# Optimization experiments

Measured on AMD Instinct MI355X. Metric: run time of the kernel, lower is better.

The kernel has to match this reference:

```python
import jax, jax.numpy as jnp
import numpy as np


def setup_inputs() -> dict:
    key = jax.random.key(0)
    k = jax.random.split(key, 6)
    B, C = 16, 256
    Hd, Wd = 32, 32   # deeper (lower-res) spatial
    Hs, Ws = 64, 64   # shallower (higher-res) spatial
    deeper = jax.random.normal(k[0], (B, C, Hd, Wd), dtype=jnp.float32)
    shallower = jax.random.normal(k[1], (B, C, Hs, Ws), dtype=jnp.float32)
    # 1x1 conv weights stored as dense matrices (kernel spatial dims are 1)
    w1 = jax.random.normal(k[2], (C, 2 * C), dtype=jnp.float32) * (1.0 / np.sqrt(2 * C))
    b1 = jnp.zeros((C,), dtype=jnp.float32)
    w2 = jax.random.normal(k[3], (C, C), dtype=jnp.float32) * (1.0 / np.sqrt(C))
    b2 = jnp.zeros((C,), dtype=jnp.float32)
    return {"deeper": deeper, "shallower": shallower, "w1": w1, "b1": b1, "w2": w2, "b2": b2}


def reference(deeper, shallower, w1, b1, w2, b2):
    # Global average pools (adaptive_avg_pool2d to 1x1) -> [B, C]
    shallow_pool = jnp.mean(shallower, axis=(2, 3))
    deeper_pool = jnp.mean(deeper, axis=(2, 3))  # deepest=False branch
    # Channel-wise concat -> [B, 2C]
    global_pool = jnp.concatenate([shallow_pool, deeper_pool], axis=1)
    # conv1x1 -> ReLU (LeakyReLU slope 0.0) -> conv1x1, on 1x1 spatial = dense matmuls
    h = jax.nn.relu(jnp.einsum('bi,oi->bo', global_pool, w1) + b1)
    gate = jnp.einsum('bi,oi->bo', h, w2) + b2  # [B, C]
    # Sigmoid channel gating broadcast over spatial dims
    gated = shallower * jax.nn.sigmoid(gate)[:, :, None, None]
    # Bilinear upsample deeper to shallower resolution (align_corners=False)
    B, C, Hs, Ws = shallower.shape
    up = jax.image.resize(deeper, (B, C, Hs, Ws), method='bilinear')
    return gated + up
```

## Files before the change

### kernel.cpp

```cpp
#include <hip/hip_runtime.h>
#include <math.h>


__global__ __launch_bounds__(256) void pool_kernel(const float* __restrict__ deeper,
                                                   const float* __restrict__ shallower,
                                                   float* __restrict__ gp) {
    const int bc = blockIdx.x;
    const int t = threadIdx.x;
    const float4* ssrc = (const float4*)(shallower + (size_t)bc * 4096);
    const float4* dsrc = (const float4*)(deeper + (size_t)bc * 1024);
    float4 a = ssrc[t], b4 = ssrc[t + 256], c4 = ssrc[t + 512], d4 = ssrc[t + 768];
    float4 e = dsrc[t];
    float s_sh = (a.x + a.y + a.z + a.w) + (b4.x + b4.y + b4.z + b4.w)
               + (c4.x + c4.y + c4.z + c4.w) + (d4.x + d4.y + d4.z + d4.w);
    float s_dp = e.x + e.y + e.z + e.w;
    #pragma unroll
    for (int off = 32; off > 0; off >>= 1) {
        s_sh += __shfl_down(s_sh, off, 64);
        s_dp += __shfl_down(s_dp, off, 64);
    }
    __shared__ float red_sh[4], red_dp[4];
    if ((t & 63) == 0) { red_sh[t >> 6] = s_sh; red_dp[t >> 6] = s_dp; }
    __syncthreads();
    if (t == 0) {
        const int bb = bc >> 8, cc = bc & 255;
        gp[bb * 512 + cc]       = (red_sh[0]+red_sh[1]+red_sh[2]+red_sh[3]) * (1.0f / 4096.0f);
        gp[bb * 512 + 256 + cc] = (red_dp[0]+red_dp[1]+red_dp[2]+red_dp[3]) * (1.0f / 1024.0f);
    }
}

__global__ __launch_bounds__(256) void mlp1_kernel(const float* __restrict__ gp,
                                                   const float* __restrict__ w1,
                                                   const float* __restrict__ b1,
                                                   float* __restrict__ h) {
    const int j = blockIdx.x;
    const int t = threadIdx.x;
    const int half = t >> 7;
    const int b = (t >> 3) & 15;
    const int o = j * 8 + (t & 7);
    const float4* gv = (const float4*)(gp + b * 512 + half * 256);
    const float4* wv = (const float4*)(w1 + (size_t)o * 512 + half * 256);
    float acc = 0.0f;
    #pragma unroll 8
    for (int i = 0; i < 64; ++i) {
        float4 g = gv[i], w = wv[i];
        acc += g.x * w.x + g.y * w.y + g.z * w.z + g.w * w.w;
    }
    __shared__ float part[256];
    part[t] = acc;
    __syncthreads();
    if (t < 128) h[b * 256 + o] = fmaxf(part[t] + part[t + 128] + b1[o], 0.0f);
}

__global__ __launch_bounds__(256) void out_kernel(const float* __restrict__ deeper,
                                                  const float* __restrict__ shallower,
                                                  const float* __restrict__ h,
                                                  const float* __restrict__ w2,
                                                  const float* __restrict__ b2,
                                                  float* __restrict__ out) {
    const int bc = blockIdx.x;
    const int b = bc >> 8, c = bc & 255;
    const int t = threadIdx.x;
    __shared__ float tile[32 * 36];
    __shared__ float red[4];
    __shared__ float sv_s;
    {
        float4 v = ((const float4*)(deeper + (size_t)bc * 1024))[t];
        const int row = t >> 3, col4 = t & 7;
        *(float4*)(tile + row * 36 + col4 * 4) = v;
    }
    {
        float p = h[b * 256 + t] * w2[(size_t)c * 256 + t];
        #pragma unroll
        for (int off = 32; off > 0; off >>= 1) p += __shfl_down(p, off, 64);
        if ((t & 63) == 0) red[t >> 6] = p;
    }
    __syncthreads();
    if (t == 0) {
        const float dot = red[0] + red[1] + red[2] + red[3] + b2[c];
        sv_s = 1.0f / (1.0f + expf(-dot));
    }
    __syncthreads();
    const float s = sv_s;
    const float4* ssrc = (const float4*)(shallower + (size_t)bc * 4096);
    float4* dst = (float4*)(out + (size_t)bc * 4096);
    #pragma unroll
    for (int j = 0; j < 4; ++j) {
        const int f4 = t + j * 256;
        const int y = f4 >> 4;
        const int m = f4 & 15;
        const int yy = 2 * y - 1;
        const int yl = yy >> 2;
        const float wy = (float)(yy & 3) * 0.25f;
        const float wy1 = 1.0f - wy;
        const int y0 = yl < 0 ? 0 : yl;
        const int y1 = (yl + 1) > 31 ? 31 : (yl + 1);
        const float* r0 = tile + y0 * 36;
        const float* r1 = tile + y1 * 36;
        const int xa = (2 * m - 1) < 0 ? 0 : (2 * m - 1);
        const int xd = (2 * m + 2) > 31 ? 31 : (2 * m + 2);
        const float A  = r0[xa]        * wy1 + r1[xa]        * wy;
        const float Bv = r0[2 * m]     * wy1 + r1[2 * m]     * wy;
        const float Cv = r0[2 * m + 1] * wy1 + r1[2 * m + 1] * wy;
        const float D  = r0[xd]        * wy1 + r1[xd]        * wy;
        float4 sh = ssrc[f4];
        float4 o;
        o.x = fmaf(sh.x, s, 0.25f * A  + 0.75f * Bv);
        o.y = fmaf(sh.y, s, 0.75f * Bv + 0.25f * Cv);
        o.z = fmaf(sh.z, s, 0.25f * Bv + 0.75f * Cv);
        o.w = fmaf(sh.w, s, 0.75f * Cv + 0.25f * D);
        dst[f4] = o;
    }
}

extern "C" void kernel_launch(void* const* d_in, const int* in_sizes, int n_in,
                              void* d_out, int out_size, void* d_ws, size_t ws_size,
                              hipStream_t stream) {
    const float* deeper    = (const float*)d_in[0];
    const float* shallower = (const float*)d_in[1];
    const float* w1        = (const float*)d_in[2];
    const float* b1        = (const float*)d_in[3];
    const float* w2        = (const float*)d_in[4];
    const float* b2        = (const float*)d_in[5];
    float* outp = (float*)d_out;

    float* gp = (float*)d_ws;
    float* h  = gp + 16 * 512;

    hipLaunchKernelGGL(pool_kernel, dim3(4096), dim3(256), 0, stream, deeper, shallower, gp);
    hipLaunchKernelGGL(mlp1_kernel, dim3(32), dim3(256), 0, stream, gp, w1, b1, h);
    hipLaunchKernelGGL(out_kernel, dim3(4096), dim3(256), 0, stream,
                       deeper, shallower, h, w2, b2, outp);
}
```

Baseline: 51.96 us.

## Spread MLP1 over more blocks, prefetch shallower loads, use nontemporal output stores

```diff
diff --git a/kernel.cpp b/kernel.cpp
--- a/kernel.cpp
+++ b/kernel.cpp
@@ -1,6 +1,8 @@
 #include <hip/hip_runtime.h>
 #include <math.h>
 
+
+typedef float f32x4_t __attribute__((ext_vector_type(4)));
 
 __global__ __launch_bounds__(256) void pool_kernel(const float* __restrict__ deeper,
                                                    const float* __restrict__ shallower,
@@ -33,23 +35,26 @@
                                                    const float* __restrict__ w1,
                                                    const float* __restrict__ b1,
                                                    float* __restrict__ h) {
-    const int j = blockIdx.x;
+    const int o = blockIdx.x;
     const int t = threadIdx.x;
-    const int half = t >> 7;
-    const int b = (t >> 3) & 15;
-    const int o = j * 8 + (t & 7);
-    const float4* gv = (const float4*)(gp + b * 512 + half * 256);
-    const float4* wv = (const float4*)(w1 + (size_t)o * 512 + half * 256);
+    const int b = t >> 4, kc = t & 15;
+    const float4* gv = (const float4*)(gp + b * 512 + kc * 32);
+    const float4* wv = (const float4*)(w1 + (size_t)o * 512 + kc * 32);
     float acc = 0.0f;
-    #pragma unroll 8
-    for (int i = 0; i < 64; ++i) {
+    #pragma unroll
+    for (int i = 0; i < 8; ++i) {
         float4 g = gv[i], w = wv[i];
         acc += g.x * w.x + g.y * w.y + g.z * w.z + g.w * w.w;
     }
     __shared__ float part[256];
     part[t] = acc;
     __syncthreads();
-    if (t < 128) h[b * 256 + o] = fmaxf(part[t] + part[t + 128] + b1[o], 0.0f);
+    if (t < 16) {
+        float v = 0.0f;
+        #pragma unroll
+        for (int k = 0; k < 16; ++k) v += part[t * 16 + k];
+        h[t * 256 + o] = fmaxf(v + b1[o], 0.0f);
+    }
 }
 
 __global__ __launch_bounds__(256) void out_kernel(const float* __restrict__ deeper,
@@ -64,6 +69,13 @@
     __shared__ float tile[32 * 36];
     __shared__ float red[4];
     __shared__ float sv_s;
+
+    const float4* ssrc = (const float4*)(shallower + (size_t)bc * 4096);
+    float4 sh0 = ssrc[t];
+    float4 sh1 = ssrc[t + 256];
+    float4 sh2 = ssrc[t + 512];
+    float4 sh3 = ssrc[t + 768];
+
     {
         float4 v = ((const float4*)(deeper + (size_t)bc * 1024))[t];
         const int row = t >> 3, col4 = t & 7;
@@ -82,8 +94,8 @@
     }
     __syncthreads();
     const float s = sv_s;
-    const float4* ssrc = (const float4*)(shallower + (size_t)bc * 4096);
-    float4* dst = (float4*)(out + (size_t)bc * 4096);
+    f32x4_t* dst = (f32x4_t*)(out + (size_t)bc * 4096);
+    float4 shv[4] = { sh0, sh1, sh2, sh3 };
     #pragma unroll
     for (int j = 0; j < 4; ++j) {
         const int f4 = t + j * 256;
@@ -103,13 +115,13 @@
         const float Bv = r0[2 * m]     * wy1 + r1[2 * m]     * wy;
         const float Cv = r0[2 * m + 1] * wy1 + r1[2 * m + 1] * wy;
         const float D  = r0[xd]        * wy1 + r1[xd]        * wy;
-        float4 sh = ssrc[f4];
-        float4 o;
+        float4 sh = shv[j];
+        f32x4_t o;
         o.x = fmaf(sh.x, s, 0.25f * A  + 0.75f * Bv);
         o.y = fmaf(sh.y, s, 0.75f * Bv + 0.25f * Cv);
         o.z = fmaf(sh.z, s, 0.25f * Bv + 0.75f * Cv);
         o.w = fmaf(sh.w, s, 0.75f * Cv + 0.25f * D);
-        dst[f4] = o;
+        __builtin_nontemporal_store(o, &dst[f4]);
     }
 }
 
@@ -128,7 +140,7 @@
     float* h  = gp + 16 * 512;
 
     hipLaunchKernelGGL(pool_kernel, dim3(4096), dim3(256), 0, stream, deeper, shallower, gp);
-    hipLaunchKernelGGL(mlp1_kernel, dim3(32), dim3(256), 0, stream, gp, w1, b1, h);
+    hipLaunchKernelGGL(mlp1_kernel, dim3(256), dim3(256), 0, stream, gp, w1, b1, h);
     hipLaunchKernelGGL(out_kernel, dim3(4096), dim3(256), 0, stream,
                        deeper, shallower, h, w2, b2, outp);
 }
```

After: 44.31 us. 1.17x faster.
